# Performance work log

Hardware: AMD Instinct MI355X
Metric: run time of the kernel (lower is better)

Reference implementation:

```python
import jax, jax.numpy as jnp
import numpy as np

B, S, D, H = 8, 2048, 1024, 64

def setup_inputs() -> dict:
    key = jax.random.key(0)
    k1, k2, k3, k4 = jax.random.split(key, 4)
    scale = 1.0 / np.sqrt(D)
    return {
        "x": jax.random.normal(k1, (B, S, D), dtype=jnp.float32),
        "Wq": jax.random.normal(k2, (D, H), dtype=jnp.float32) * scale,
        "Wk": jax.random.normal(k3, (D, H), dtype=jnp.float32) * scale,
        "Wv": jax.random.normal(k4, (D, H), dtype=jnp.float32) * scale,
    }

def reference(x, Wq, Wk, Wv):
    # QKV projections (no bias)
    Q = jnp.einsum('bsd,dh->bsh', x, Wq)
    K = jnp.einsum('bsd,dh->bsh', x, Wk)
    V = jnp.einsum('bsd,dh->bsh', x, Wv)
    seq_len = x.shape[1]
    head_dim = Wq.shape[1]
    # full [B, S, S] score matrix, scaled by sqrt(head_dim)
    scores = jnp.einsum('bqh,bkh->bqk', Q, K) / jnp.sqrt(jnp.asarray(head_dim, x.dtype))
    # causal mask: positions j > i masked to -inf
    causal = jnp.tril(jnp.ones((seq_len, seq_len), dtype=bool))
    scores = jnp.where(causal[None, :, :], scores, -jnp.inf)
    probs = jax.nn.softmax(scores, axis=-1)
    return jnp.einsum('bqk,bkh->bqh', probs, V)
```

## Files before the change

### kernel.cpp

```cpp
#include <hip/hip_runtime.h>
#include <math.h>

#define B_ 8
#define S_ 2048
#define D_ 1024
#define H_ 64
#define BS_ (B_ * S_)

typedef __attribute__((ext_vector_type(8))) short bf16x8;
typedef __attribute__((ext_vector_type(4))) float f32x4;

static __device__ __forceinline__ short f2bf(float f) {
    unsigned u = __builtin_bit_cast(unsigned, f);
    u = (u + 0x7fffu + ((u >> 16) & 1u)) >> 16;
    return (short)u;
}


__global__ __launch_bounds__(256) void wprep(
    const float* __restrict__ Wq, const float* __restrict__ Wk,
    const float* __restrict__ Wv, short* __restrict__ Wt)
{
    const int o  = blockIdx.x >> 4;
    const int k0 = (blockIdx.x & 15) * 64;
    const float* __restrict__ W = (o == 0) ? Wq : ((o == 1) ? Wk : Wv);
    const float scale = (o == 0) ? 0.125f * 1.44269504088896340736f : 1.0f;

    __shared__ float ls[64][65];
    const int r = threadIdx.x >> 6;
    const int c = threadIdx.x & 63;

    #pragma unroll
    for (int i = 0; i < 16; ++i)
        ls[i * 4 + r][c] = W[(size_t)(k0 + i * 4 + r) * H_ + c];
    __syncthreads();
    #pragma unroll
    for (int i = 0; i < 16; ++i) {
        const int n = i * 4 + r;
        Wt[(size_t)(o * 64 + n) * D_ + k0 + c] = f2bf(ls[c][n] * scale);
    }
}

__global__ __launch_bounds__(256) void qkv_proj(
    const float* __restrict__ x, const short* __restrict__ Wt,
    short* __restrict__ Qp, short* __restrict__ Kp, short* __restrict__ Vp)
{
    __shared__ short xs[32][136];
    __shared__ short wsh[192][136];

    const int t = threadIdx.x;
    const int w = t >> 6, lane = t & 63, col = lane & 15, quad = lane >> 4;
    const int row0 = blockIdx.x * 32;
    const int xrow = t >> 3;
    const int xkc  = (t & 7) * 16;

    f32x4 acc[2][3] = {};

    float4 xf[4];
    bf16x8 wf[12];
    auto load_tile = [&](int k0) {
        #pragma unroll
        for (int i = 0; i < 4; ++i)
            xf[i] = *(const float4*)&x[(size_t)(row0 + xrow) * D_ + k0 + xkc + i * 4];
        #pragma unroll
        for (int i = 0; i < 12; ++i) {
            const int idx = t + i * 256;
            wf[i] = *(const bf16x8*)&Wt[(size_t)(idx >> 4) * D_ + k0 + (idx & 15) * 8];
        }
    };

    load_tile(0);
    for (int k0 = 0; k0 < D_; k0 += 128) {
        #pragma unroll
        for (int h = 0; h < 2; ++h) {
            const float4 f0 = xf[h * 2], f1 = xf[h * 2 + 1];
            bf16x8 av;
            av[0] = f2bf(f0.x); av[1] = f2bf(f0.y); av[2] = f2bf(f0.z); av[3] = f2bf(f0.w);
            av[4] = f2bf(f1.x); av[5] = f2bf(f1.y); av[6] = f2bf(f1.z); av[7] = f2bf(f1.w);
            *(bf16x8*)&xs[xrow][xkc + h * 8] = av;
        }
        #pragma unroll
        for (int i = 0; i < 12; ++i) {
            const int idx = t + i * 256;
            *(bf16x8*)&wsh[idx >> 4][(idx & 15) * 8] = wf[i];
        }
        __syncthreads();
        if (k0 + 128 < D_) load_tile(k0 + 128);

        #pragma unroll
        for (int ks = 0; ks < 4; ++ks) {
            const int ka = ks * 32 + quad * 8;
            bf16x8 a0 = *(const bf16x8*)&xs[col][ka];
            bf16x8 a1 = *(const bf16x8*)&xs[16 + col][ka];
            #pragma unroll
            for (int nt = 0; nt < 3; ++nt) {
                bf16x8 bfr = *(const bf16x8*)&wsh[w * 48 + nt * 16 + col][ka];
                acc[0][nt] = __builtin_amdgcn_mfma_f32_16x16x32_bf16(a0, bfr, acc[0][nt], 0, 0, 0);
                acc[1][nt] = __builtin_amdgcn_mfma_f32_16x16x32_bf16(a1, bfr, acc[1][nt], 0, 0, 0);
            }
        }
        __syncthreads();
    }

    short (*Cs)[200] = (short(*)[200])&wsh[0][0];
    #pragma unroll
    for (int mt = 0; mt < 2; ++mt)
        #pragma unroll
        for (int nt = 0; nt < 3; ++nt)
            #pragma unroll
            for (int r = 0; r < 4; ++r)
                Cs[mt * 16 + quad * 4 + r][w * 48 + nt * 16 + col] = f2bf(acc[mt][nt][r]);
    __syncthreads();

    const int qtile = row0 >> 4;
    const int ktg   = row0 >> 6;
    const int half  = (row0 >> 5) & 1;

    if (w < 2) {
        #pragma unroll
        for (int f = 0; f < 2; ++f) {
            bf16x8 v = *(const bf16x8*)&Cs[w * 16 + col][f * 32 + quad * 8];
            *(bf16x8*)&Qp[((size_t)(qtile + w) * 2 + f) * 512 + lane * 8] = v;
        }
    } else {
        const int ks = w - 2;
        #pragma unroll
        for (int ntl = 0; ntl < 2; ++ntl) {
            const int nt = half * 2 + ntl;
            bf16x8 v = *(const bf16x8*)&Cs[ntl * 16 + col][64 + ks * 32 + quad * 8];
            *(bf16x8*)&Kp[((size_t)(ktg * 4 + nt) * 2 + ks) * 512 + lane * 8] = v;
        }
    }
    {
        const int nt = w;
        bf16x8 v;
        #pragma unroll
        for (int jj = 0; jj < 8; ++jj)
            v[jj] = Cs[quad * 8 + jj][128 + nt * 16 + col];
        *(bf16x8*)&Vp[((size_t)(ktg * 2 + half) * 4 + nt) * 512 + lane * 8] = v;
    }
}

__global__ __launch_bounds__(256) void attn(
    const short* __restrict__ Qp, const short* __restrict__ Kp,
    const short* __restrict__ Vp, float* __restrict__ outp)
{
    __shared__ short Ps[4][16][72];
    __shared__ float pO[3][16][68];
    __shared__ float pml[2][3][16];

    const int bi = blockIdx.x;
    const int j  = 127 - (bi >> 3);
    const int b  = bi & 7;
    const int t  = threadIdx.x;
    const int w = t >> 6, lane = t & 63, col = lane & 15, quad = lane >> 4;
    const int qbase = j * 16;
    const int nkt = (j + 4) >> 2;
    const int gbase = b * 32;

    const short* Qpb = Qp + ((size_t)(b * 128 + j) * 2) * 512;
    const bf16x8 aq0 = *(const bf16x8*)&Qpb[lane * 8];
    const bf16x8 aq1 = *(const bf16x8*)&Qpb[512 + lane * 8];

    f32x4 Oacc[4] = {};
    float m[4] = {-INFINITY, -INFINITY, -INFINITY, -INFINITY};
    float l[4] = {0.f, 0.f, 0.f, 0.f};

    auto load_K = [&](bf16x8 (&dst)[4][2], int g) {
        const short* base = Kp + (size_t)g * 4096;
        #pragma unroll
        for (int nt = 0; nt < 4; ++nt) {
            dst[nt][0] = *(const bf16x8*)&base[nt * 1024 + lane * 8];
            dst[nt][1] = *(const bf16x8*)&base[nt * 1024 + 512 + lane * 8];
        }
    };

    bf16x8 kc[4][2], kn[4][2];
    if (w < nkt) load_K(kc, gbase + w);

    for (int kt = w; kt < nkt; kt += 4) {
        const int kbase = kt * 64;
        const bool more = (kt + 4) < nkt;
        if (more) load_K(kn, gbase + kt + 4);

        f32x4 S[4] = {};
        #pragma unroll
        for (int nt = 0; nt < 4; ++nt) {
            S[nt] = __builtin_amdgcn_mfma_f32_16x16x32_bf16(aq0, kc[nt][0], S[nt], 0, 0, 0);
            S[nt] = __builtin_amdgcn_mfma_f32_16x16x32_bf16(aq1, kc[nt][1], S[nt], 0, 0, 0);
        }

        const short* vb = Vp + (size_t)(gbase + kt) * 4096;
        bf16x8 vv[2][4];
        #pragma unroll
        for (int ks = 0; ks < 2; ++ks)
            #pragma unroll
            for (int nt = 0; nt < 4; ++nt)
                vv[ks][nt] = *(const bf16x8*)&vb[(ks * 4 + nt) * 512 + lane * 8];

        if (kbase + 63 > qbase) {
            #pragma unroll
            for (int nt = 0; nt < 4; ++nt) {
                const int key = kbase + nt * 16 + col;
                #pragma unroll
                for (int r = 0; r < 4; ++r)
                    if (key > qbase + quad * 4 + r) S[nt][r] = -INFINITY;
            }
        }

        float alpha[4];
        #pragma unroll
        for (int r = 0; r < 4; ++r) {
            float mx = fmaxf(fmaxf(S[0][r], S[1][r]), fmaxf(S[2][r], S[3][r]));
            mx = fmaxf(mx, __shfl_xor(mx, 1));
            mx = fmaxf(mx, __shfl_xor(mx, 2));
            mx = fmaxf(mx, __shfl_xor(mx, 4));
            mx = fmaxf(mx, __shfl_xor(mx, 8));
            const float mn = fmaxf(m[r], mx);
            alpha[r] = __builtin_amdgcn_exp2f(m[r] - mn);
            m[r] = mn;
            float rs = 0.f;
            #pragma unroll
            for (int nt = 0; nt < 4; ++nt) {
                const float p = __builtin_amdgcn_exp2f(S[nt][r] - mn);
                S[nt][r] = p;
                rs += p;
            }
            rs += __shfl_xor(rs, 1);
            rs += __shfl_xor(rs, 2);
            rs += __shfl_xor(rs, 4);
            rs += __shfl_xor(rs, 8);
            l[r] = l[r] * alpha[r] + rs;
        }
        #pragma unroll
        for (int nt = 0; nt < 4; ++nt)
            #pragma unroll
            for (int r = 0; r < 4; ++r) Oacc[nt][r] *= alpha[r];

        #pragma unroll
        for (int nt = 0; nt < 4; ++nt)
            #pragma unroll
            for (int r = 0; r < 4; ++r)
                Ps[w][quad * 4 + r][nt * 16 + col] = f2bf(S[nt][r]);
        __asm__ volatile("s_waitcnt lgkmcnt(0)" ::: "memory");

        #pragma unroll
        for (int ks = 0; ks < 2; ++ks) {
            bf16x8 ap = *(const bf16x8*)&Ps[w][col][ks * 32 + quad * 8];
            #pragma unroll
            for (int nt = 0; nt < 4; ++nt)
                Oacc[nt] = __builtin_amdgcn_mfma_f32_16x16x32_bf16(ap, vv[ks][nt], Oacc[nt], 0, 0, 0);
        }

        if (more) {
            #pragma unroll
            for (int nt = 0; nt < 4; ++nt) {
                kc[nt][0] = kn[nt][0];
                kc[nt][1] = kn[nt][1];
            }
        }
    }

    __syncthreads();
    if (w > 0) {
        #pragma unroll
        for (int nt = 0; nt < 4; ++nt)
            #pragma unroll
            for (int r = 0; r < 4; ++r)
                pO[w - 1][quad * 4 + r][nt * 16 + col] = Oacc[nt][r];
        if (col == 0) {
            #pragma unroll
            for (int r = 0; r < 4; ++r) {
                pml[0][w - 1][quad * 4 + r] = m[r];
                pml[1][w - 1][quad * 4 + r] = l[r];
            }
        }
    }
    __syncthreads();
    if (w == 0) {
        #pragma unroll
        for (int r = 0; r < 4; ++r) {
            const int row = quad * 4 + r;
            float M = m[r];
            #pragma unroll
            for (int i = 0; i < 3; ++i) M = fmaxf(M, pml[0][i][row]);
            const float a0 = __builtin_amdgcn_exp2f(m[r] - M);
            float ai[3];
            float L = a0 * l[r];
            #pragma unroll
            for (int i = 0; i < 3; ++i) {
                ai[i] = __builtin_amdgcn_exp2f(pml[0][i][row] - M);
                L += ai[i] * pml[1][i][row];
            }
            const float inv = 1.0f / L;
            float* dst = outp + (size_t)(b * S_ + qbase + row) * H_;
            #pragma unroll
            for (int nt = 0; nt < 4; ++nt) {
                float v = a0 * Oacc[nt][r];
                #pragma unroll
                for (int i = 0; i < 3; ++i) v += ai[i] * pO[i][row][nt * 16 + col];
                dst[nt * 16 + col] = v * inv;
            }
        }
    }
}

extern "C" void kernel_launch(void* const* d_in, const int* in_sizes, int n_in,
                              void* d_out, int out_size, void* d_ws, size_t ws_size,
                              hipStream_t stream)
{
    const float* x  = (const float*)d_in[0];
    const float* Wq = (const float*)d_in[1];
    const float* Wk = (const float*)d_in[2];
    const float* Wv = (const float*)d_in[3];
    float* out = (float*)d_out;

    short* Qp = (short*)d_ws;
    short* Kp = Qp + (size_t)BS_ * H_;
    short* Vp = Kp + (size_t)BS_ * H_;
    short* Wt = Vp + (size_t)BS_ * H_;

    hipLaunchKernelGGL(wprep,    dim3(48), dim3(256), 0, stream, Wq, Wk, Wv, Wt);
    hipLaunchKernelGGL(qkv_proj, dim3(BS_ / 32), dim3(256), 0, stream, x, Wt, Qp, Kp, Vp);
    hipLaunchKernelGGL(attn,     dim3(B_ * (S_ / 16)), dim3(256), 0, stream, Qp, Kp, Vp, out);
}
```

Before: 130.8 us.

## Pre-pack weights into MFMA fragment layout and stream them from registers in QKV projection

The weight prep kernel now writes Wq/Wk/Wv directly in per-lane MFMA B-fragment order. The projection kernel stages the whole 32-row x block as bf16 in LDS once, then loops over K with double-buffered register loads of weights straight from global memory. This removes the per-tile weight LDS staging and the two barriers per K step. The attention kernel also drops the separate next-K register buffer and reloads K in place after the QK MFMAs, which lowers register pressure but leaves less prefetch distance.

```diff
diff --git a/kernel.cpp b/kernel.cpp
--- a/kernel.cpp
+++ b/kernel.cpp
@@ -8,6 +8,7 @@
 #define BS_ (B_ * S_)
 
 typedef __attribute__((ext_vector_type(8))) short bf16x8;
+typedef __attribute__((ext_vector_type(4))) short bf16x4;
 typedef __attribute__((ext_vector_type(4))) float f32x4;
 
 static __device__ __forceinline__ short f2bf(float f) {
@@ -19,90 +20,88 @@
 
 __global__ __launch_bounds__(256) void wprep(
     const float* __restrict__ Wq, const float* __restrict__ Wk,
-    const float* __restrict__ Wv, short* __restrict__ Wt)
+    const float* __restrict__ Wv, short* __restrict__ Wfp)
 {
-    const int o  = blockIdx.x >> 4;
-    const int k0 = (blockIdx.x & 15) * 64;
-    const float* __restrict__ W = (o == 0) ? Wq : ((o == 1) ? Wk : Wv);
-    const float scale = (o == 0) ? 0.125f * 1.44269504088896340736f : 1.0f;
-
-    __shared__ float ls[64][65];
-    const int r = threadIdx.x >> 6;
-    const int c = threadIdx.x & 63;
-
+    const int ks = blockIdx.x;
+    __shared__ float ws[3][32][68];
+
+    const int t = threadIdx.x;
+    const int r  = t >> 3;
+    const int c0 = (t & 7) * 8;
     #pragma unroll
-    for (int i = 0; i < 16; ++i)
-        ls[i * 4 + r][c] = W[(size_t)(k0 + i * 4 + r) * H_ + c];
-    __syncthreads();
+    for (int o = 0; o < 3; ++o) {
+        const float* __restrict__ W = (o == 0) ? Wq : ((o == 1) ? Wk : Wv);
+        *(float4*)&ws[o][r][c0]     = *(const float4*)&W[(size_t)(ks * 32 + r) * H_ + c0];
+        *(float4*)&ws[o][r][c0 + 4] = *(const float4*)&W[(size_t)(ks * 32 + r) * H_ + c0 + 4];
+    }
+    __syncthreads();
+
+    const int w = t >> 6, lane = t & 63, col = lane & 15, quad = lane >> 4;
     #pragma unroll
-    for (int i = 0; i < 16; ++i) {
-        const int n = i * 4 + r;
-        Wt[(size_t)(o * 64 + n) * D_ + k0 + c] = f2bf(ls[c][n] * scale);
+    for (int i = 0; i < 3; ++i) {
+        const int fid = i * 4 + w;
+        const int o = fid >> 2, ntl = fid & 3;
+        const float scale = (o == 0) ? 0.125f * 1.4426950408889634f : 1.0f;
+        bf16x8 v;
+        #pragma unroll
+        for (int j = 0; j < 8; ++j)
+            v[j] = f2bf(ws[o][quad * 8 + j][ntl * 16 + col] * scale);
+        *(bf16x8*)&Wfp[((size_t)fid * 32 + ks) * 512 + lane * 8] = v;
     }
 }
 
 __global__ __launch_bounds__(256) void qkv_proj(
-    const float* __restrict__ x, const short* __restrict__ Wt,
+    const float* __restrict__ x, const short* __restrict__ Wfp,
     short* __restrict__ Qp, short* __restrict__ Kp, short* __restrict__ Vp)
 {
-    __shared__ short xs[32][136];
-    __shared__ short wsh[192][136];
+    __shared__ short xs[32][1032];
 
     const int t = threadIdx.x;
     const int w = t >> 6, lane = t & 63, col = lane & 15, quad = lane >> 4;
     const int row0 = blockIdx.x * 32;
-    const int xrow = t >> 3;
-    const int xkc  = (t & 7) * 16;
+
+    #pragma unroll
+    for (int rr = 0; rr < 32; ++rr) {
+        float4 f = *(const float4*)&x[(size_t)(row0 + rr) * D_ + t * 4];
+        bf16x4 v;
+        v[0] = f2bf(f.x); v[1] = f2bf(f.y); v[2] = f2bf(f.z); v[3] = f2bf(f.w);
+        *(bf16x4*)&xs[rr][t * 4] = v;
+    }
+
+    const short* __restrict__ wb = Wfp + (size_t)(w * 3) * 32 * 512 + lane * 8;
+
+    bf16x8 wfb[2][3];
+    auto load_W = [&](bf16x8 (&d)[3], int ks) {
+        #pragma unroll
+        for (int i = 0; i < 3; ++i)
+            d[i] = *(const bf16x8*)&wb[((size_t)i * 32 + ks) * 512];
+    };
+    load_W(wfb[0], 0);
+    load_W(wfb[1], 1);
+
+    __syncthreads();
+
+    bf16x8 xab[2][2];
+    auto load_A = [&](bf16x8 (&d)[2], int ks) {
+        d[0] = *(const bf16x8*)&xs[col][ks * 32 + quad * 8];
+        d[1] = *(const bf16x8*)&xs[16 + col][ks * 32 + quad * 8];
+    };
+    load_A(xab[0], 0);
 
     f32x4 acc[2][3] = {};
-
-    float4 xf[4];
-    bf16x8 wf[12];
-    auto load_tile = [&](int k0) {
-        #pragma unroll
-        for (int i = 0; i < 4; ++i)
-            xf[i] = *(const float4*)&x[(size_t)(row0 + xrow) * D_ + k0 + xkc + i * 4];
-        #pragma unroll
-        for (int i = 0; i < 12; ++i) {
-            const int idx = t + i * 256;
-            wf[i] = *(const bf16x8*)&Wt[(size_t)(idx >> 4) * D_ + k0 + (idx & 15) * 8];
-        }
-    };
-
-    load_tile(0);
-    for (int k0 = 0; k0 < D_; k0 += 128) {
-        #pragma unroll
-        for (int h = 0; h < 2; ++h) {
-            const float4 f0 = xf[h * 2], f1 = xf[h * 2 + 1];
-            bf16x8 av;
-            av[0] = f2bf(f0.x); av[1] = f2bf(f0.y); av[2] = f2bf(f0.z); av[3] = f2bf(f0.w);
-            av[4] = f2bf(f1.x); av[5] = f2bf(f1.y); av[6] = f2bf(f1.z); av[7] = f2bf(f1.w);
-            *(bf16x8*)&xs[xrow][xkc + h * 8] = av;
-        }
-        #pragma unroll
-        for (int i = 0; i < 12; ++i) {
-            const int idx = t + i * 256;
-            *(bf16x8*)&wsh[idx >> 4][(idx & 15) * 8] = wf[i];
-        }
-        __syncthreads();
-        if (k0 + 128 < D_) load_tile(k0 + 128);
-
-        #pragma unroll
-        for (int ks = 0; ks < 4; ++ks) {
-            const int ka = ks * 32 + quad * 8;
-            bf16x8 a0 = *(const bf16x8*)&xs[col][ka];
-            bf16x8 a1 = *(const bf16x8*)&xs[16 + col][ka];
-            #pragma unroll
-            for (int nt = 0; nt < 3; ++nt) {
-                bf16x8 bfr = *(const bf16x8*)&wsh[w * 48 + nt * 16 + col][ka];
-                acc[0][nt] = __builtin_amdgcn_mfma_f32_16x16x32_bf16(a0, bfr, acc[0][nt], 0, 0, 0);
-                acc[1][nt] = __builtin_amdgcn_mfma_f32_16x16x32_bf16(a1, bfr, acc[1][nt], 0, 0, 0);
-            }
-        }
-        __syncthreads();
-    }
-
-    short (*Cs)[200] = (short(*)[200])&wsh[0][0];
+    for (int ks = 0; ks < 32; ++ks) {
+        const int cur = ks & 1;
+        if (ks + 1 < 32) load_A(xab[cur ^ 1], ks + 1);
+        #pragma unroll
+        for (int nt = 0; nt < 3; ++nt) {
+            acc[0][nt] = __builtin_amdgcn_mfma_f32_16x16x32_bf16(xab[cur][0], wfb[cur][nt], acc[0][nt], 0, 0, 0);
+            acc[1][nt] = __builtin_amdgcn_mfma_f32_16x16x32_bf16(xab[cur][1], wfb[cur][nt], acc[1][nt], 0, 0, 0);
+        }
+        if (ks + 2 < 32) load_W(wfb[cur], ks + 2);
+    }
+
+    __syncthreads();
+    short (*Cs)[200] = (short(*)[200])&xs[0][0];
     #pragma unroll
     for (int mt = 0; mt < 2; ++mt)
         #pragma unroll
@@ -175,13 +174,11 @@
         }
     };
 
-    bf16x8 kc[4][2], kn[4][2];
+    bf16x8 kc[4][2];
     if (w < nkt) load_K(kc, gbase + w);
 
     for (int kt = w; kt < nkt; kt += 4) {
         const int kbase = kt * 64;
-        const bool more = (kt + 4) < nkt;
-        if (more) load_K(kn, gbase + kt + 4);
 
         f32x4 S[4] = {};
         #pragma unroll
@@ -189,6 +186,8 @@
             S[nt] = __builtin_amdgcn_mfma_f32_16x16x32_bf16(aq0, kc[nt][0], S[nt], 0, 0, 0);
             S[nt] = __builtin_amdgcn_mfma_f32_16x16x32_bf16(aq1, kc[nt][1], S[nt], 0, 0, 0);
         }
+
+        if (kt + 4 < nkt) load_K(kc, gbase + kt + 4);
 
         const short* vb = Vp + (size_t)(gbase + kt) * 4096;
         bf16x8 vv[2][4];
@@ -251,14 +250,6 @@
             for (int nt = 0; nt < 4; ++nt)
                 Oacc[nt] = __builtin_amdgcn_mfma_f32_16x16x32_bf16(ap, vv[ks][nt], Oacc[nt], 0, 0, 0);
         }
-
-        if (more) {
-            #pragma unroll
-            for (int nt = 0; nt < 4; ++nt) {
-                kc[nt][0] = kn[nt][0];
-                kc[nt][1] = kn[nt][1];
-            }
-        }
     }
 
     __syncthreads();
@@ -315,12 +306,12 @@
     const float* Wv = (const float*)d_in[3];
     float* out = (float*)d_out;
 
-    short* Qp = (short*)d_ws;
-    short* Kp = Qp + (size_t)BS_ * H_;
-    short* Vp = Kp + (size_t)BS_ * H_;
-    short* Wt = Vp + (size_t)BS_ * H_;
-
-    hipLaunchKernelGGL(wprep,    dim3(48), dim3(256), 0, stream, Wq, Wk, Wv, Wt);
-    hipLaunchKernelGGL(qkv_proj, dim3(BS_ / 32), dim3(256), 0, stream, x, Wt, Qp, Kp, Vp);
+    short* Qp  = (short*)d_ws;
+    short* Kp  = Qp + (size_t)BS_ * H_;
+    short* Vp  = Kp + (size_t)BS_ * H_;
+    short* Wfp = Vp + (size_t)BS_ * H_;
+
+    hipLaunchKernelGGL(wprep,    dim3(32), dim3(256), 0, stream, Wq, Wk, Wv, Wfp);
+    hipLaunchKernelGGL(qkv_proj, dim3(BS_ / 32), dim3(256), 0, stream, x, Wfp, Qp, Kp, Vp);
     hipLaunchKernelGGL(attn,     dim3(B_ * (S_ / 16)), dim3(256), 0, stream, Qp, Kp, Vp, out);
 }
```

New measurement: 123.6 us. -5.5%, faster.
